# Performance work log

Measured on AMD Instinct MI355X. Metric: run time of the kernel, lower is better.

## Reference

```python
import jax, jax.numpy as jnp
import numpy as np

NEG_SLOPE = 0.2
LN_EPS = 1e-6

B, L, D, H = 32, 512, 256, 4
N = B * L
E = 65536
C = D  # per-head out channels (GATConv out_channels=d_model)


def setup_inputs() -> dict:
    key = jax.random.key(0)
    ks = jax.random.split(key, 10)
    s = 1.0 / np.sqrt(D)
    inputs = jax.random.normal(ks[0], (B, L, D), dtype=jnp.float32)
    edge_index = jax.random.randint(ks[1], (2, E), 0, N, dtype=jnp.int64)
    return {
        "inputs": inputs,
        "edge_index": edge_index,
        "ln_gamma": jnp.ones((D,), jnp.float32),
        "ln_beta": jnp.zeros((D,), jnp.float32),
        "W1": jax.random.normal(ks[2], (D, D), jnp.float32) * s,   # linear_before_gnn
        "b1": jnp.zeros((D,), jnp.float32),
        "W_gat": jax.random.normal(ks[3], (H * C, D), jnp.float32) * s,  # GATConv.lin (no bias)
        "att_src": jax.random.normal(ks[4], (H, C), jnp.float32) * s,
        "att_dst": jax.random.normal(ks[5], (H, C), jnp.float32) * s,
        "bias_gat": jnp.zeros((C,), jnp.float32),  # concat=False -> size out_channels
        "W2": jax.random.normal(ks[6], (D, D), jnp.float32) * s,   # linear_after_gnn
        "b2": jnp.zeros((D,), jnp.float32),
    }


def _gat_conv(x, edge_index, W_gat, att_src, att_dst, bias_gat):
    # x: [N, D] -> project to [N, H, C]
    xh = (x @ W_gat.T).reshape(N, H, C)
    # add self loops (PyG default add_self_loops=True)
    loops = jnp.arange(N, dtype=edge_index.dtype)
    src = jnp.concatenate([edge_index[0], loops])  # message source j
    dst = jnp.concatenate([edge_index[1], loops])  # message target i
    # per-node attention logits [N, H]
    a_src = jnp.einsum("nhc,hc->nh", xh, att_src)
    a_dst = jnp.einsum("nhc,hc->nh", xh, att_dst)
    # per-edge logits and segment softmax over destination node
    e = jax.nn.leaky_relu(a_src[src] + a_dst[dst], NEG_SLOPE)  # [Etot, H]
    e_max = jax.ops.segment_max(e, dst, num_segments=N)        # every node has a self loop
    e = jnp.exp(e - e_max[dst])
    denom = jax.ops.segment_sum(e, dst, num_segments=N)
    alpha = e / denom[dst]                                     # [Etot, H]
    # weighted message aggregation (dropout on alpha skipped: eval mode)
    msg = xh[src] * alpha[:, :, None]                          # [Etot, H, C]
    out = jax.ops.segment_sum(msg, dst, num_segments=N)        # [N, H, C]
    return out.mean(axis=1) + bias_gat                         # concat=False -> head mean


def reference(inputs, edge_index, ln_gamma, ln_beta, W1, b1, W_gat, att_src, att_dst, bias_gat, W2, b2):
    # LayerNorm(eps=1e-6)
    mu = inputs.mean(-1, keepdims=True)
    var = jnp.mean((inputs - mu) ** 2, axis=-1, keepdims=True)
    x = (inputs - mu) * jax.lax.rsqrt(var + LN_EPS) * ln_gamma + ln_beta
    x = x.reshape(-1, D)
    gnn_in = x @ W1.T + b1
    gnn_out = _gat_conv(gnn_in, edge_index, W_gat, att_src, att_dst, bias_gat)
    y = gnn_out @ W2.T + b2
    # dropout is identity in eval mode; residual add
    return y.reshape(B, L, D) + inputs
```

## Files before the change

kernel.cpp:

```cpp
#include <hip/hip_runtime.h>
#include <math.h>

#define N_NODES 16384
#define D_MODEL 256
#define H_HEADS 4
#define C_CH 256
#define E_EDGES 65536
#define ETOT (E_EDGES + N_NODES)
#define HC 1024
#define MAXDEG 64

typedef __bf16 bf16x8 __attribute__((ext_vector_type(8)));
typedef __bf16 bf16x4 __attribute__((ext_vector_type(4)));
typedef float f32x4 __attribute__((ext_vector_type(4)));

__device__ __forceinline__ __bf16 f2bf(float f) { return (__bf16)f; }
__device__ __forceinline__ float bf2f(__bf16 b) { return (float)b; }

__global__ __launch_bounds__(256) void prep1_ln(
    const float* __restrict__ Wg, const float* __restrict__ att_src,
    const float* __restrict__ att_dst, const float* __restrict__ W2,
    const int* __restrict__ ei, const float* __restrict__ in,
    const float* __restrict__ gamma, const float* __restrict__ beta,
    float* __restrict__ t, float* __restrict__ V, int* __restrict__ cnt,
    int* __restrict__ csr, __bf16* __restrict__ x_ln)
{
    int b = blockIdx.x;
    int tid = threadIdx.x;
    if (b >= 2432) {
        int wave = tid >> 6, lane = tid & 63;
        int row = (b - 2432) * 4 + wave;
        float4 v = ((const float4*)(in + (size_t)row * D_MODEL))[lane];
        float s  = v.x + v.y + v.z + v.w;
        float sq = v.x*v.x + v.y*v.y + v.z*v.z + v.w*v.w;
        for (int off = 32; off; off >>= 1) {
            s  += __shfl_xor(s,  off);
            sq += __shfl_xor(sq, off);
        }
        float mean = s * (1.0f / D_MODEL);
        float var  = sq * (1.0f / D_MODEL) - mean * mean;
        float inv  = rsqrtf(var + 1e-6f);
        float4 g = ((const float4*)gamma)[lane];
        float4 bb = ((const float4*)beta)[lane];
        bf16x4 o;
        o[0] = f2bf((v.x - mean) * inv * g.x + bb.x);
        o[1] = f2bf((v.y - mean) * inv * g.y + bb.y);
        o[2] = f2bf((v.z - mean) * inv * g.z + bb.z);
        o[3] = f2bf((v.w - mean) * inv * g.w + bb.w);
        *(bf16x4*)(x_ln + (size_t)row * D_MODEL + lane * 4) = o;
        return;
    }
    if (b < 64) {
        int v = b >> 3, sl = b & 7, h = v & 3;
        const float* att = ((v < 4) ? att_src : att_dst) + h * C_CH;
        float acc = 0.f;
        #pragma unroll
        for (int j = 0; j < 32; ++j) {
            int c = sl * 32 + j;
            acc = fmaf(Wg[(size_t)(h * 256 + c) * 256 + tid], att[c], acc);
        }
        atomicAdd(&t[v * 256 + tid], acc);
        return;
    }
    if (b < 2112) {
        int bb2 = b - 64;
        int orig = bb2 >> 3, cs = bb2 & 7;
        int og = (orig & 63) * 4, h = orig >> 6;
        const float* w2r = W2 + (size_t)og * 256;
        const float* wgp = Wg + ((size_t)h * 256) * 256 + tid;
        float a0 = 0.f, a1 = 0.f, a2 = 0.f, a3 = 0.f;
        int cb = cs * 32;
        #pragma unroll 4
        for (int c = cb; c < cb + 32; ++c) {
            float wv = wgp[(size_t)c * 256];
            a0 = fmaf(w2r[c],       wv, a0);
            a1 = fmaf(w2r[256 + c], wv, a1);
            a2 = fmaf(w2r[512 + c], wv, a2);
            a3 = fmaf(w2r[768 + c], wv, a3);
        }
        size_t base = (size_t)og * 1024 + h * 256 + tid;
        atomicAdd(&V[base],        a0);
        atomicAdd(&V[base + 1024], a1);
        atomicAdd(&V[base + 2048], a2);
        atomicAdd(&V[base + 3072], a3);
        return;
    }
    {
        int e = (b - 2112) * 256 + tid;
        int src, dst;
        if (e < E_EDGES) { src = ei[e]; dst = ei[E_EDGES + e]; }
        else             { src = dst = e - E_EDGES; }
        int pos = atomicAdd(cnt + dst, 1);
        csr[(size_t)dst * MAXDEG + pos] = src;
    }
}

__global__ __launch_bounds__(256) void prep2(
    const float* __restrict__ t, const float* __restrict__ W1,
    const float* __restrict__ b1, const float* __restrict__ V,
    const float* __restrict__ W2, const float* __restrict__ bg,
    const float* __restrict__ b2, float* __restrict__ u2,
    float* __restrict__ c0, float* __restrict__ Wzf,
    float* __restrict__ bias_z)
{
    __shared__ float red[4][4];
    int b = blockIdx.x;
    int d = threadIdx.x;

    if (b < 2048) {
        int orig = b >> 3, ks = b & 7;
        int og = (orig & 63) * 4, h = orig >> 6;
        int lane = d & 63, wid = d >> 6;
        const float* vr = V + (size_t)og * 1024 + h * 256;
        float a0 = 0.f, a1 = 0.f, a2 = 0.f, a3 = 0.f;
        int kb = ks * 32;
        #pragma unroll 4
        for (int k = kb; k < kb + 32; ++k) {
            float w1v = W1[(size_t)k * 256 + d];
            a0 = fmaf(vr[k],        w1v, a0);
            a1 = fmaf(vr[1024 + k], w1v, a1);
            a2 = fmaf(vr[2048 + k], w1v, a2);
            a3 = fmaf(vr[3072 + k], w1v, a3);
        }
        size_t base = (size_t)og * 1024 + h * 256 + d;
        atomicAdd(&Wzf[base],        a0);
        atomicAdd(&Wzf[base + 1024], a1);
        atomicAdd(&Wzf[base + 2048], a2);
        atomicAdd(&Wzf[base + 3072], a3);

        if (ks == 0) {
            float b1v = b1[d];
            #pragma unroll
            for (int j = 0; j < 4; ++j) {
                float p = vr[(size_t)j * 1024 + d] * b1v;
                for (int s = 32; s; s >>= 1) p += __shfl_xor(p, s);
                if (lane == 0) red[j][wid] = p;
            }
            __syncthreads();
            if (d < 4) {
                float s = red[d][0] + red[d][1] + red[d][2] + red[d][3];
                atomicAdd(&bias_z[og + d], 0.25f * s);
            }
            if (h == 0) {
                __syncthreads();
                float bgv = bg[d];
                #pragma unroll
                for (int j = 0; j < 4; ++j) {
                    float q = W2[(size_t)(og + j) * 256 + d] * bgv;
                    for (int s = 32; s; s >>= 1) q += __shfl_xor(q, s);
                    if (lane == 0) red[j][wid] = q;
                }
                __syncthreads();
                if (d < 4) {
                    float s = red[d][0] + red[d][1] + red[d][2] + red[d][3];
                    atomicAdd(&bias_z[og + d], s + b2[og + d]);
                }
            }
        }
        return;
    }
    {
        int bb = b - 2048;
        int v = bb >> 3, sl = bb & 7;
        const float* tv = t + v * 256;
        float acc = 0.f;
        #pragma unroll
        for (int j = 0; j < 32; ++j) {
            int k = sl * 32 + j;
            acc = fmaf(tv[k], W1[(size_t)k * 256 + d], acc);
        }
        atomicAdd(&u2[v * 256 + d], acc);
        if (d < 32) {
            float p = tv[sl * 32 + d] * b1[sl * 32 + d];
            for (int s = 16; s; s >>= 1) p += __shfl_xor(p, s);
            if (d == 0) atomicAdd(&c0[v], p);
        }
    }
}

__global__ __launch_bounds__(256) void logits_cvt(
    const __bf16* __restrict__ x_ln, const float* __restrict__ u2,
    const float* __restrict__ c0, float* __restrict__ a_src,
    float* __restrict__ a_dst, const float* __restrict__ Wzf,
    __bf16* __restrict__ Wz)
{
    int b = blockIdx.x;
    int tid = threadIdx.x;
    if (b >= 4096) {
        int idx = (b - 4096) * 256 + tid;
        float4 v = ((const float4*)Wzf)[idx];
        bf16x4 o;
        o[0] = f2bf(v.x); o[1] = f2bf(v.y); o[2] = f2bf(v.z); o[3] = f2bf(v.w);
        *(bf16x4*)(Wz + (size_t)idx * 4) = o;
        return;
    }
    __shared__ float u2s[8][256];
    __shared__ float c0s[8];
    #pragma unroll
    for (int k = 0; k < 8; ++k) u2s[k][tid] = u2[k * 256 + tid];
    if (tid < 8) c0s[tid] = c0[tid];
    __syncthreads();

    int wave = tid >> 6, lane = tid & 63;
    int n = b * 4 + wave;
    int v = lane >> 3, p = lane & 7;
    const __bf16* xp = x_ln + (size_t)n * D_MODEL + p * 32;
    const float*  up = &u2s[v][p * 32];
    float acc = 0.f;
    #pragma unroll
    for (int ti = 0; ti < 4; ++ti) {
        bf16x8 x = *(const bf16x8*)(xp + ti * 8);
        #pragma unroll
        for (int j = 0; j < 8; ++j)
            acc = fmaf(bf2f(x[j]), up[ti * 8 + j], acc);
    }
    acc += __shfl_xor(acc, 1);
    acc += __shfl_xor(acc, 2);
    acc += __shfl_xor(acc, 4);
    if (p == 0) {
        float o = acc + c0s[v];
        if (v < 4) a_src[n * H_HEADS + v] = o;
        else       a_dst[n * H_HEADS + (v - 4)] = o;
    }
}

__global__ __launch_bounds__(256) void gat_fused(
    const __bf16* __restrict__ x_ln, const float* __restrict__ a_src,
    const float* __restrict__ a_dst, const int* __restrict__ cnt,
    const int* __restrict__ csr, __bf16* __restrict__ agg)
{
    int wave = threadIdx.x >> 6, lane = threadIdx.x & 63;
    int i = blockIdx.x * 4 + wave;
    int deg = cnt[i];
    int sidx = csr[(size_t)i * MAXDEG + lane];
    float4 ad = *(const float4*)(a_dst + i * H_HEADS);

    float acc[4][4] = {};
    float sm0 = 0.f, sm1 = 0.f, sm2 = 0.f, sm3 = 0.f;

    int e = 0;
    for (; e + 4 <= deg; e += 4) {
        int s0 = __shfl(sidx, e);
        int s1 = __shfl(sidx, e + 1);
        int s2 = __shfl(sidx, e + 2);
        int s3 = __shfl(sidx, e + 3);
        float4 A0 = *(const float4*)(a_src + s0 * H_HEADS);
        float4 A1 = *(const float4*)(a_src + s1 * H_HEADS);
        float4 A2 = *(const float4*)(a_src + s2 * H_HEADS);
        float4 A3 = *(const float4*)(a_src + s3 * H_HEADS);
        bf16x4 X0 = *(const bf16x4*)(x_ln + (size_t)s0 * D_MODEL + lane * 4);
        bf16x4 X1 = *(const bf16x4*)(x_ln + (size_t)s1 * D_MODEL + lane * 4);
        bf16x4 X2 = *(const bf16x4*)(x_ln + (size_t)s2 * D_MODEL + lane * 4);
        bf16x4 X3 = *(const bf16x4*)(x_ln + (size_t)s3 * D_MODEL + lane * 4);

        float l[4][4] = {
            {A0.x + ad.x, A0.y + ad.y, A0.z + ad.z, A0.w + ad.w},
            {A1.x + ad.x, A1.y + ad.y, A1.z + ad.z, A1.w + ad.w},
            {A2.x + ad.x, A2.y + ad.y, A2.z + ad.z, A2.w + ad.w},
            {A3.x + ad.x, A3.y + ad.y, A3.z + ad.z, A3.w + ad.w}};
        float wgt[4][4];
        #pragma unroll
        for (int q = 0; q < 4; ++q)
            #pragma unroll
            for (int h = 0; h < 4; ++h) {
                float lv = l[q][h];
                lv = (lv > 0.f) ? lv : 0.2f * lv;
                wgt[q][h] = __expf(lv);
            }
        sm0 += wgt[0][0] + wgt[1][0] + wgt[2][0] + wgt[3][0];
        sm1 += wgt[0][1] + wgt[1][1] + wgt[2][1] + wgt[3][1];
        sm2 += wgt[0][2] + wgt[1][2] + wgt[2][2] + wgt[3][2];
        sm3 += wgt[0][3] + wgt[1][3] + wgt[2][3] + wgt[3][3];
        #pragma unroll
        for (int j = 0; j < 4; ++j) {
            float x0 = bf2f(X0[j]), x1 = bf2f(X1[j]);
            float x2 = bf2f(X2[j]), x3 = bf2f(X3[j]);
            #pragma unroll
            for (int h = 0; h < 4; ++h) {
                float a = acc[h][j];
                a = fmaf(wgt[0][h], x0, a);
                a = fmaf(wgt[1][h], x1, a);
                a = fmaf(wgt[2][h], x2, a);
                a = fmaf(wgt[3][h], x3, a);
                acc[h][j] = a;
            }
        }
    }
    for (; e < deg; ++e) {
        int s = __shfl(sidx, e);
        float4 as = *(const float4*)(a_src + s * H_HEADS);
        bf16x4 x = *(const bf16x4*)(x_ln + (size_t)s * D_MODEL + lane * 4);
        float l0 = as.x + ad.x, l1 = as.y + ad.y,
              l2 = as.z + ad.z, l3 = as.w + ad.w;
        l0 = (l0 > 0.f) ? l0 : 0.2f * l0;
        l1 = (l1 > 0.f) ? l1 : 0.2f * l1;
        l2 = (l2 > 0.f) ? l2 : 0.2f * l2;
        l3 = (l3 > 0.f) ? l3 : 0.2f * l3;
        float w0 = __expf(l0), w1 = __expf(l1);
        float w2 = __expf(l2), w3 = __expf(l3);
        sm0 += w0; sm1 += w1; sm2 += w2; sm3 += w3;
        #pragma unroll
        for (int j = 0; j < 4; ++j) {
            float xv = bf2f(x[j]);
            acc[0][j] = fmaf(w0, xv, acc[0][j]);
            acc[1][j] = fmaf(w1, xv, acc[1][j]);
            acc[2][j] = fmaf(w2, xv, acc[2][j]);
            acc[3][j] = fmaf(w3, xv, acc[3][j]);
        }
    }
    float sc[4] = {0.25f / sm0, 0.25f / sm1, 0.25f / sm2, 0.25f / sm3};
    #pragma unroll
    for (int h = 0; h < 4; ++h) {
        bf16x4 o;
        #pragma unroll
        for (int j = 0; j < 4; ++j) o[j] = f2bf(acc[h][j] * sc[h]);
        *(bf16x4*)(agg + (size_t)i * HC + h * 256 + lane * 4) = o;
    }
}

#define APAD 72

__global__ __launch_bounds__(256) void gemm_skinny(
    const __bf16* __restrict__ A, const __bf16* __restrict__ B,
    const float* __restrict__ bias, const float* __restrict__ resid,
    float* __restrict__ outf, int K)
{
    __shared__ __align__(16) __bf16 As[64 * APAD];
    __shared__ __align__(16) __bf16 Bs[256 * APAD];
    int tid  = threadIdx.x;
    int lane = tid & 63;
    int w    = tid >> 6;
    int quad = lane >> 4;
    int l16  = lane & 15;
    int m0 = blockIdx.x * 64;
    int n0 = w * 64;

    int srow = tid >> 3, sp = tid & 7;
    const __bf16* Ab = A + (size_t)(m0 + srow) * K + sp * 8;
    const __bf16* Bb = B + (size_t)srow * K + sp * 8;
    size_t rstride = (size_t)32 * K;

    f32x4 acc[4][4] = {};

    bf16x8 a0_0, a0_1, b0_[8];
    bf16x8 a1_0, a1_1, b1_[8];

    auto compute = [&]() {
        #pragma unroll
        for (int ks = 0; ks < 2; ++ks) {
            bf16x8 af[4], bfr[4];
            #pragma unroll
            for (int mt = 0; mt < 4; ++mt)
                af[mt] = *(const bf16x8*)(As + (mt * 16 + l16) * APAD
                                          + ks * 32 + quad * 8);
            #pragma unroll
            for (int nt = 0; nt < 4; ++nt)
                bfr[nt] = *(const bf16x8*)(Bs + (n0 + nt * 16 + l16) * APAD
                                           + ks * 32 + quad * 8);
            #pragma unroll
            for (int mt = 0; mt < 4; ++mt)
                #pragma unroll
                for (int nt = 0; nt < 4; ++nt)
                    acc[mt][nt] = __builtin_amdgcn_mfma_f32_16x16x32_bf16(
                        af[mt], bfr[nt], acc[mt][nt], 0, 0, 0);
        }
    };

    a0_0 = *(const bf16x8*)(Ab);
    a0_1 = *(const bf16x8*)(Ab + rstride);
    #pragma unroll
    for (int t = 0; t < 8; ++t)
        b0_[t] = *(const bf16x8*)(Bb + t * rstride);

    for (int kb = 0; kb < K; kb += 128) {
        {
            const __bf16* Ap = Ab + kb + 64;
            const __bf16* Bp = Bb + kb + 64;
            a1_0 = *(const bf16x8*)(Ap);
            a1_1 = *(const bf16x8*)(Ap + rstride);
            #pragma unroll
            for (int t = 0; t < 8; ++t)
                b1_[t] = *(const bf16x8*)(Bp + t * rstride);
        }
        __syncthreads();
        *(bf16x8*)(As + srow * APAD + sp * 8)        = a0_0;
        *(bf16x8*)(As + (srow + 32) * APAD + sp * 8) = a0_1;
        #pragma unroll
        for (int t = 0; t < 8; ++t)
            *(bf16x8*)(Bs + (srow + t * 32) * APAD + sp * 8) = b0_[t];
        __syncthreads();
        compute();

        if (kb + 128 < K) {
            const __bf16* Ap = Ab + kb + 128;
            const __bf16* Bp = Bb + kb + 128;
            a0_0 = *(const bf16x8*)(Ap);
            a0_1 = *(const bf16x8*)(Ap + rstride);
            #pragma unroll
            for (int t = 0; t < 8; ++t)
                b0_[t] = *(const bf16x8*)(Bp + t * rstride);
        }
        __syncthreads();
        *(bf16x8*)(As + srow * APAD + sp * 8)        = a1_0;
        *(bf16x8*)(As + (srow + 32) * APAD + sp * 8) = a1_1;
        #pragma unroll
        for (int t = 0; t < 8; ++t)
            *(bf16x8*)(Bs + (srow + t * 32) * APAD + sp * 8) = b1_[t];
        __syncthreads();
        compute();
    }

    #pragma unroll
    for (int nt = 0; nt < 4; ++nt) {
        int col = n0 + nt * 16 + l16;
        float bv = bias[col];
        #pragma unroll
        for (int mt = 0; mt < 4; ++mt) {
            int row = m0 + mt * 16 + quad * 4;
            #pragma unroll
            for (int r = 0; r < 4; ++r) {
                size_t off = (size_t)(row + r) * C_CH + col;
                outf[off] = acc[mt][nt][r] + bv + resid[off];
            }
        }
    }
}

extern "C" void kernel_launch(void* const* d_in, const int* in_sizes, int n_in,
                              void* d_out, int out_size, void* d_ws, size_t ws_size,
                              hipStream_t stream)
{
    const float* inp      = (const float*)d_in[0];
    const int*   ei       = (const int*)  d_in[1];
    const float* ln_gamma = (const float*)d_in[2];
    const float* ln_beta  = (const float*)d_in[3];
    const float* W1       = (const float*)d_in[4];
    const float* b1       = (const float*)d_in[5];
    const float* W_gat    = (const float*)d_in[6];
    const float* att_src  = (const float*)d_in[7];
    const float* att_dst  = (const float*)d_in[8];
    const float* bias_gat = (const float*)d_in[9];
    const float* W2       = (const float*)d_in[10];
    const float* b2       = (const float*)d_in[11];

    char* ws = (char*)d_ws;
    __bf16* x_ln_bf = (__bf16*)(ws);
    __bf16* agg_bf  = (__bf16*)(ws + (8ull  << 20));
    __bf16* Wz_b    = (__bf16*)(ws + (40ull << 20));
    float*  a_src_b = (float*)(ws + (41ull << 20));
    float*  a_dst_b = a_src_b + (size_t)N_NODES * H_HEADS;
    float*  t_vec   = (float*)(ws + (42ull << 20));
    float*  u2      = t_vec + 2048;
    float*  c0      = u2 + 2048;
    float*  bias_z  = c0 + 8;
    int*    cnt     = (int*)(bias_z + 256);
    float*  V_f     = (float*)(cnt + N_NODES);
    float*  Wzf     = V_f + 256 * 1024;
    int*    csr     = (int*)(ws + (45ull << 20));

    size_t zbytes = (2048 + 2048 + 8 + 256) * sizeof(float)
                  + N_NODES * sizeof(int)
                  + 2 * 256 * 1024 * sizeof(float);
    hipMemsetAsync(t_vec, 0, zbytes, stream);

    prep1_ln<<<2432 + 4096, 256, 0, stream>>>(W_gat, att_src, att_dst, W2, ei,
                                              inp, ln_gamma, ln_beta,
                                              t_vec, V_f, cnt, csr, x_ln_bf);
    prep2<<<2112, 256, 0, stream>>>(t_vec, W1, b1, V_f, W2, bias_gat, b2,
                                    u2, c0, Wzf, bias_z);
    logits_cvt<<<4096 + 256, 256, 0, stream>>>(x_ln_bf, u2, c0,
                                               a_src_b, a_dst_b, Wzf, Wz_b);
    gat_fused<<<N_NODES / 4, 256, 0, stream>>>(x_ln_bf, a_src_b, a_dst_b,
                                               cnt, csr, agg_bf);
    gemm_skinny<<<N_NODES / 64, 256, 0, stream>>>(agg_bf, Wz_b, bias_z, inp,
                                                  (float*)d_out, HC);
}
```

Baseline: 163.6 us.

## Replace float atomics with split-K partial buffers and widen final GEMM to 8 waves

The split-K weight-folding products (V and Wz) now write per-slice partial buffers instead of using atomicAdd, and later stages sum the 8 partials. This removes atomic contention and shrinks the memset, at the cost of extra memory traffic for the 8x partial reads. Separately, the final skinny GEMM now runs 512 threads per block, each wave covering 32 output columns, to raise parallelism and cut per-thread register use.

```diff
diff --git a/kernel.cpp b/kernel.cpp
--- a/kernel.cpp
+++ b/kernel.cpp
@@ -9,6 +9,7 @@
 #define ETOT (E_EDGES + N_NODES)
 #define HC 1024
 #define MAXDEG 64
+#define PSZ 262144
 
 typedef __bf16 bf16x8 __attribute__((ext_vector_type(8)));
 typedef __bf16 bf16x4 __attribute__((ext_vector_type(4)));
@@ -22,7 +23,7 @@
     const float* __restrict__ att_dst, const float* __restrict__ W2,
     const int* __restrict__ ei, const float* __restrict__ in,
     const float* __restrict__ gamma, const float* __restrict__ beta,
-    float* __restrict__ t, float* __restrict__ V, int* __restrict__ cnt,
+    float* __restrict__ t, float* __restrict__ Vp, int* __restrict__ cnt,
     int* __restrict__ csr, __bf16* __restrict__ x_ln)
 {
     int b = blockIdx.x;
@@ -78,11 +79,11 @@
             a2 = fmaf(w2r[512 + c], wv, a2);
             a3 = fmaf(w2r[768 + c], wv, a3);
         }
-        size_t base = (size_t)og * 1024 + h * 256 + tid;
-        atomicAdd(&V[base],        a0);
-        atomicAdd(&V[base + 1024], a1);
-        atomicAdd(&V[base + 2048], a2);
-        atomicAdd(&V[base + 3072], a3);
+        size_t base = (size_t)cs * PSZ + (size_t)og * 1024 + h * 256 + tid;
+        Vp[base]        = a0;
+        Vp[base + 1024] = a1;
+        Vp[base + 2048] = a2;
+        Vp[base + 3072] = a3;
         return;
     }
     {
@@ -97,13 +98,14 @@
 
 __global__ __launch_bounds__(256) void prep2(
     const float* __restrict__ t, const float* __restrict__ W1,
-    const float* __restrict__ b1, const float* __restrict__ V,
+    const float* __restrict__ b1, const float* __restrict__ Vp,
     const float* __restrict__ W2, const float* __restrict__ bg,
     const float* __restrict__ b2, float* __restrict__ u2,
-    float* __restrict__ c0, float* __restrict__ Wzf,
+    float* __restrict__ c0, float* __restrict__ Wzp,
     float* __restrict__ bias_z)
 {
     __shared__ float red[4][4];
+    __shared__ float vsh[4][32];
     int b = blockIdx.x;
     int d = threadIdx.x;
 
@@ -111,28 +113,43 @@
         int orig = b >> 3, ks = b & 7;
         int og = (orig & 63) * 4, h = orig >> 6;
         int lane = d & 63, wid = d >> 6;
-        const float* vr = V + (size_t)og * 1024 + h * 256;
+        int kb = ks * 32;
+        size_t vbase = (size_t)og * 1024 + h * 256;
+
+        if (d < 128) {
+            int j = d >> 5, kk = d & 31;
+            float s = 0.f;
+            #pragma unroll
+            for (int cs = 0; cs < 8; ++cs)
+                s += Vp[(size_t)cs * PSZ + vbase + (size_t)j * 1024 + kb + kk];
+            vsh[j][kk] = s;
+        }
+        __syncthreads();
+
         float a0 = 0.f, a1 = 0.f, a2 = 0.f, a3 = 0.f;
-        int kb = ks * 32;
         #pragma unroll 4
-        for (int k = kb; k < kb + 32; ++k) {
-            float w1v = W1[(size_t)k * 256 + d];
-            a0 = fmaf(vr[k],        w1v, a0);
-            a1 = fmaf(vr[1024 + k], w1v, a1);
-            a2 = fmaf(vr[2048 + k], w1v, a2);
-            a3 = fmaf(vr[3072 + k], w1v, a3);
-        }
-        size_t base = (size_t)og * 1024 + h * 256 + d;
-        atomicAdd(&Wzf[base],        a0);
-        atomicAdd(&Wzf[base + 1024], a1);
-        atomicAdd(&Wzf[base + 2048], a2);
-        atomicAdd(&Wzf[base + 3072], a3);
+        for (int k = 0; k < 32; ++k) {
+            float w1v = W1[(size_t)(kb + k) * 256 + d];
+            a0 = fmaf(vsh[0][k], w1v, a0);
+            a1 = fmaf(vsh[1][k], w1v, a1);
+            a2 = fmaf(vsh[2][k], w1v, a2);
+            a3 = fmaf(vsh[3][k], w1v, a3);
+        }
+        size_t base = (size_t)ks * PSZ + vbase + d;
+        Wzp[base]        = a0;
+        Wzp[base + 1024] = a1;
+        Wzp[base + 2048] = a2;
+        Wzp[base + 3072] = a3;
 
         if (ks == 0) {
             float b1v = b1[d];
             #pragma unroll
             for (int j = 0; j < 4; ++j) {
-                float p = vr[(size_t)j * 1024 + d] * b1v;
+                float vsum = 0.f;
+                #pragma unroll
+                for (int cs = 0; cs < 8; ++cs)
+                    vsum += Vp[(size_t)cs * PSZ + vbase + (size_t)j * 1024 + d];
+                float p = vsum * b1v;
                 for (int s = 32; s; s >>= 1) p += __shfl_xor(p, s);
                 if (lane == 0) red[j][wid] = p;
             }
@@ -181,14 +198,19 @@
 __global__ __launch_bounds__(256) void logits_cvt(
     const __bf16* __restrict__ x_ln, const float* __restrict__ u2,
     const float* __restrict__ c0, float* __restrict__ a_src,
-    float* __restrict__ a_dst, const float* __restrict__ Wzf,
+    float* __restrict__ a_dst, const float* __restrict__ Wzp,
     __bf16* __restrict__ Wz)
 {
     int b = blockIdx.x;
     int tid = threadIdx.x;
     if (b >= 4096) {
         int idx = (b - 4096) * 256 + tid;
-        float4 v = ((const float4*)Wzf)[idx];
+        float4 v = make_float4(0.f, 0.f, 0.f, 0.f);
+        #pragma unroll
+        for (int p = 0; p < 8; ++p) {
+            float4 t4 = ((const float4*)(Wzp + (size_t)p * PSZ))[idx];
+            v.x += t4.x; v.y += t4.y; v.z += t4.z; v.w += t4.w;
+        }
         bf16x4 o;
         o[0] = f2bf(v.x); o[1] = f2bf(v.y); o[2] = f2bf(v.z); o[3] = f2bf(v.w);
         *(bf16x4*)(Wz + (size_t)idx * 4) = o;
@@ -320,7 +342,7 @@
 
 #define APAD 72
 
-__global__ __launch_bounds__(256) void gemm_skinny(
+__global__ __launch_bounds__(512) void gemm_skinny(
     const __bf16* __restrict__ A, const __bf16* __restrict__ B,
     const float* __restrict__ bias, const float* __restrict__ resid,
     float* __restrict__ outf, int K)
@@ -333,85 +355,80 @@
     int quad = lane >> 4;
     int l16  = lane & 15;
     int m0 = blockIdx.x * 64;
-    int n0 = w * 64;
+    int n0 = w * 32;
 
     int srow = tid >> 3, sp = tid & 7;
     const __bf16* Ab = A + (size_t)(m0 + srow) * K + sp * 8;
     const __bf16* Bb = B + (size_t)srow * K + sp * 8;
-    size_t rstride = (size_t)32 * K;
-
-    f32x4 acc[4][4] = {};
-
-    bf16x8 a0_0, a0_1, b0_[8];
-    bf16x8 a1_0, a1_1, b1_[8];
+    size_t rstride = (size_t)64 * K;
+
+    f32x4 acc[4][2] = {};
+
+    bf16x8 a0_, b0_[4];
+    bf16x8 a1_, b1_[4];
 
     auto compute = [&]() {
         #pragma unroll
         for (int ks = 0; ks < 2; ++ks) {
-            bf16x8 af[4], bfr[4];
+            bf16x8 af[4], bfr[2];
             #pragma unroll
             for (int mt = 0; mt < 4; ++mt)
                 af[mt] = *(const bf16x8*)(As + (mt * 16 + l16) * APAD
                                           + ks * 32 + quad * 8);
             #pragma unroll
-            for (int nt = 0; nt < 4; ++nt)
+            for (int nt = 0; nt < 2; ++nt)
                 bfr[nt] = *(const bf16x8*)(Bs + (n0 + nt * 16 + l16) * APAD
                                            + ks * 32 + quad * 8);
             #pragma unroll
             for (int mt = 0; mt < 4; ++mt)
                 #pragma unroll
-                for (int nt = 0; nt < 4; ++nt)
+                for (int nt = 0; nt < 2; ++nt)
                     acc[mt][nt] = __builtin_amdgcn_mfma_f32_16x16x32_bf16(
                         af[mt], bfr[nt], acc[mt][nt], 0, 0, 0);
         }
     };
 
-    a0_0 = *(const bf16x8*)(Ab);
-    a0_1 = *(const bf16x8*)(Ab + rstride);
+    a0_ = *(const bf16x8*)(Ab);
     #pragma unroll
-    for (int t = 0; t < 8; ++t)
+    for (int t = 0; t < 4; ++t)
         b0_[t] = *(const bf16x8*)(Bb + t * rstride);
 
     for (int kb = 0; kb < K; kb += 128) {
         {
             const __bf16* Ap = Ab + kb + 64;
             const __bf16* Bp = Bb + kb + 64;
-            a1_0 = *(const bf16x8*)(Ap);
-            a1_1 = *(const bf16x8*)(Ap + rstride);
-            #pragma unroll
-            for (int t = 0; t < 8; ++t)
+            a1_ = *(const bf16x8*)(Ap);
+            #pragma unroll
+            for (int t = 0; t < 4; ++t)
                 b1_[t] = *(const bf16x8*)(Bp + t * rstride);
         }
         __syncthreads();
-        *(bf16x8*)(As + srow * APAD + sp * 8)        = a0_0;
-        *(bf16x8*)(As + (srow + 32) * APAD + sp * 8) = a0_1;
-        #pragma unroll
-        for (int t = 0; t < 8; ++t)
-            *(bf16x8*)(Bs + (srow + t * 32) * APAD + sp * 8) = b0_[t];
+        *(bf16x8*)(As + srow * APAD + sp * 8) = a0_;
+        #pragma unroll
+        for (int t = 0; t < 4; ++t)
+            *(bf16x8*)(Bs + (srow + t * 64) * APAD + sp * 8) = b0_[t];
         __syncthreads();
         compute();
 
         if (kb + 128 < K) {
             const __bf16* Ap = Ab + kb + 128;
             const __bf16* Bp = Bb + kb + 128;
-            a0_0 = *(const bf16x8*)(Ap);
-            a0_1 = *(const bf16x8*)(Ap + rstride);
-            #pragma unroll
-            for (int t = 0; t < 8; ++t)
+            a0_ = *(const bf16x8*)(Ap);
+            #pragma unroll
+            for (int t = 0; t < 4; ++t)
                 b0_[t] = *(const bf16x8*)(Bp + t * rstride);
         }
         __syncthreads();
-        *(bf16x8*)(As + srow * APAD + sp * 8)        = a1_0;
-        *(bf16x8*)(As + (srow + 32) * APAD + sp * 8) = a1_1;
-        #pragma unroll
-        for (int t = 0; t < 8; ++t)
-            *(bf16x8*)(Bs + (srow + t * 32) * APAD + sp * 8) = b1_[t];
+        *(bf16x8*)(As + srow * APAD + sp * 8) = a1_;
+        #pragma unroll
+        for (int t = 0; t < 4; ++t)
+            *(bf16x8*)(Bs + (srow + t * 64) * APAD + sp * 8) = b1_[t];
         __syncthreads();
         compute();
     }
 
     #pragma unroll
-    for (int nt = 0; nt < 4; ++nt) {
+    for (int nt = 0; nt < 2; ++nt) {
         int col = n0 + nt * 16 + l16;
         float bv = bias[col];
         #pragma unroll
@@ -454,24 +471,23 @@
     float*  c0      = u2 + 2048;
     float*  bias_z  = c0 + 8;
     int*    cnt     = (int*)(bias_z + 256);
-    float*  V_f     = (float*)(cnt + N_NODES);
-    float*  Wzf     = V_f + 256 * 1024;
     int*    csr     = (int*)(ws + (45ull << 20));
+    float*  Vp      = (float*)(ws + (49ull << 20));
+    float*  Wzp     = (float*)(ws + (57ull << 20));
 
     size_t zbytes = (2048 + 2048 + 8 + 256) * sizeof(float)
-                  + N_NODES * sizeof(int)
-                  + 2 * 256 * 1024 * sizeof(float);
+                  + N_NODES * sizeof(int);
     hipMemsetAsync(t_vec, 0, zbytes, stream);
 
     prep1_ln<<<2432 + 4096, 256, 0, stream>>>(W_gat, att_src, att_dst, W2, ei,
                                               inp, ln_gamma, ln_beta,
-                                              t_vec, V_f, cnt, csr, x_ln_bf);
-    prep2<<<2112, 256, 0, stream>>>(t_vec, W1, b1, V_f, W2, bias_gat, b2,
-                                    u2, c0, Wzf, bias_z);
+                                              t_vec, Vp, cnt, csr, x_ln_bf);
+    prep2<<<2112, 256, 0, stream>>>(t_vec, W1, b1, Vp, W2, bias_gat, b2,
+                                    u2, c0, Wzp, bias_z);
     logits_cvt<<<4096 + 256, 256, 0, stream>>>(x_ln_bf, u2, c0,
-                                               a_src_b, a_dst_b, Wzf, Wz_b);
+                                               a_src_b, a_dst_b, Wzp, Wz_b);
     gat_fused<<<N_NODES / 4, 256, 0, stream>>>(x_ln_bf, a_src_b, a_dst_b,
                                                cnt, csr, agg_bf);
-    gemm_skinny<<<N_NODES / 64, 256, 0, stream>>>(agg_bf, Wz_b, bias_z, inp,
+    gemm_skinny<<<N_NODES / 64, 512, 0, stream>>>(agg_bf, Wz_b, bias_z, inp,
                                                   (float*)d_out, HC);
 }
```

Result: faster. 155.5 us (-4.9%).
